# Kernel optimization log

Hardware: AMD Instinct MI355X
Metric: run time of the kernel (lower is better)

Reference implementation:

```python
import jax, jax.numpy as jnp
import numpy as np

N = 50000   # nodes
E = 800000  # edges (before self-loops)
IN, HID, OUT = 128, 128, 64


def gcn_norm(edge_index, num_nodes):
    # add self loops with weight 1, then symmetric deg^-1/2 normalization
    loop = jnp.arange(num_nodes, dtype=edge_index.dtype)
    row = jnp.concatenate([edge_index[0], loop])
    col = jnp.concatenate([edge_index[1], loop])
    ew = jnp.ones(row.shape[0], dtype=jnp.float32)
    deg = jax.ops.segment_sum(ew, col, num_segments=num_nodes)
    dis = jnp.where(deg > 0, jax.lax.rsqrt(deg), 0.0)
    norm = dis[row] * ew * dis[col]
    return row, col, norm


def gcn_conv(x, row, col, norm, W, b):
    h = x @ W                                   # [N, F_out] dense GEMM
    msg = h[row] * norm[:, None]                # gather + scale over edges
    out = jax.ops.segment_sum(msg, col, num_segments=x.shape[0])  # scatter-add
    return out + b


def setup_inputs() -> dict:
    key = jax.random.key(0)
    k0, k1, k2, k3, k4, k5 = jax.random.split(key, 6)
    x = jax.random.normal(k0, (N, IN), dtype=jnp.float32)
    edge_index = jax.random.randint(k1, (2, E), 0, N, dtype=jnp.int32)
    # glorot-style init for linear weights, zeros for bias (PyG default)
    W1 = jax.random.normal(k2, (IN, HID), dtype=jnp.float32) * np.float32(np.sqrt(1.0 / IN))
    b1 = jnp.zeros((HID,), dtype=jnp.float32)
    W2 = jax.random.normal(k3, (HID, OUT), dtype=jnp.float32) * np.float32(np.sqrt(1.0 / HID))
    b2 = jnp.zeros((OUT,), dtype=jnp.float32)
    return {"x": x, "edge_index": edge_index, "W1": W1, "b1": b1, "W2": W2, "b2": b2}


def reference(x, edge_index, W1, b1, W2, b2):
    row, col, norm = gcn_norm(edge_index, x.shape[0])
    h = jax.nn.relu(gcn_conv(x, row, col, norm, W1, b1))
    # dropout is a no-op in eval mode (training=False)
    out = gcn_conv(h, row, col, norm, W2, b2)
    return out
```

## Files before the change

### kernel.cpp

```cpp
#include <hip/hip_runtime.h>
#include <hip/hip_fp16.h>


#define Nn 50000
#define Ne 800000
#define NE2 (Ne / 2)
#define SCAN_B ((Nn + 1023) / 1024)
#define GT32 ((Nn + 31) / 32)
#define E1B ((NE2 + 255) / 256)

using f16x8 = _Float16 __attribute__((ext_vector_type(8)));
using f32x4 = float __attribute__((ext_vector_type(4)));

__global__ __launch_bounds__(256) void k_count_prep(
    const int2* __restrict__ col2, int* __restrict__ degi,
    ushort2* __restrict__ rank2, const float* __restrict__ W1,
    const float* __restrict__ W2, _Float16* __restrict__ W1h,
    _Float16* __restrict__ W2h) {
  const int b = blockIdx.x, t = threadIdx.x;
  if (b < E1B) {
    int i0 = b * 256 + t;
    if (i0 < NE2) {
      int2 c = col2[i0];
      ushort2 rk;
      rk.x = (unsigned short)atomicAdd(&degi[c.x], 1);
      rk.y = (unsigned short)atomicAdd(&degi[c.y], 1);
      rank2[i0] = rk;
    }
  } else if (b == E1B) {
    for (int i = 0; i < 8; ++i) {
      int id = i * 256 + t;
      int c = id & 127, k8 = id >> 7;
      f16x8 hv;
      #pragma unroll
      for (int j = 0; j < 8; ++j) hv[j] = (_Float16)W1[(k8 * 8 + j) * 128 + c];
      *(f16x8*)&W1h[c * 128 + ((k8 ^ (c & 7)) << 3)] = hv;
    }
  } else {
    for (int i = 0; i < 4; ++i) {
      int id = i * 256 + t;
      int c = id & 63, k8 = id >> 6;
      f16x8 hv;
      #pragma unroll
      for (int j = 0; j < 8; ++j) hv[j] = (_Float16)W2[(k8 * 8 + j) * 64 + c];
      *(f16x8*)&W2h[c * 128 + ((k8 ^ (c & 7)) << 3)] = hv;
    }
  }
}

__global__ __launch_bounds__(1024) void k_scan1(const int* __restrict__ degi,
                                                int* __restrict__ rowptr,
                                                float* __restrict__ dis,
                                                int* __restrict__ bsum) {
  __shared__ int wsum[16];
  int tid = threadIdx.x;
  int lane = tid & 63, wid = tid >> 6;
  int i = blockIdx.x * 1024 + tid;
  int v = (i < Nn) ? degi[i] : 0;
  if (i < Nn) dis[i] = rsqrtf((float)(v + 1));
  int incl = v;
  #pragma unroll
  for (int off = 1; off < 64; off <<= 1) {
    int t = __shfl_up(incl, off);
    if (lane >= off) incl += t;
  }
  if (lane == 63) wsum[wid] = incl;
  __syncthreads();
  if (wid == 0) {
    int wv = (lane < 16) ? wsum[lane] : 0;
    #pragma unroll
    for (int off = 1; off < 16; off <<= 1) {
      int t = __shfl_up(wv, off);
      if (lane >= off) wv += t;
    }
    if (lane < 16) wsum[lane] = wv;
  }
  __syncthreads();
  int woff = (wid > 0) ? wsum[wid - 1] : 0;
  if (i < Nn) rowptr[i] = woff + incl - v;
  if (tid == 0) bsum[blockIdx.x] = wsum[15];
}

__global__ __launch_bounds__(1024) void k_scan3(int* __restrict__ rowptr,
                                                const int* __restrict__ bsum) {
  __shared__ int off_s;
  int tid = threadIdx.x;
  if (tid < 64) {
    int v = (tid < SCAN_B) ? bsum[tid] : 0;
    int incl = v;
    #pragma unroll
    for (int off = 1; off < 64; off <<= 1) {
      int t = __shfl_up(incl, off);
      if (tid >= off) incl += t;
    }
    if (tid == (int)blockIdx.x) off_s = incl - v;
    if (blockIdx.x == 0 && tid == SCAN_B - 1) rowptr[Nn] = incl;
  }
  __syncthreads();
  int i = blockIdx.x * 1024 + tid;
  if (i < Nn) rowptr[i] += off_s;
}

__global__ __launch_bounds__(256, 5) void k_gemm32_fill(
    const float* __restrict__ X, const _Float16* __restrict__ W1h,
    const float* __restrict__ dis, __half* __restrict__ H,
    const int2* __restrict__ row2, const int2* __restrict__ col2,
    const int* __restrict__ rowptr, const ushort2* __restrict__ rank2,
    unsigned short* __restrict__ csr) {
  __shared__ _Float16 Wts[128 * 128];
  _Float16* Hsx = Wts;

  const int tid = threadIdx.x;
  const int base = blockIdx.x * 32;

  {
    const f16x8* src = (const f16x8*)W1h;
    f16x8* dst = (f16x8*)Wts;
    #pragma unroll
    for (int i = 0; i < 8; ++i) dst[i * 256 + tid] = src[i * 256 + tid];
  }

  {
    int t = blockIdx.x * 256 + tid;
    if (t < NE2) {
      int2 r = row2[t];
      int2 c = col2[t];
      ushort2 k = rank2[t];
      csr[rowptr[c.x] + (int)k.x] = (unsigned short)r.x;
      csr[rowptr[c.y] + (int)k.y] = (unsigned short)r.y;
    }
  }

  const int w = tid >> 6, lane = tid & 63;
  const int quad = lane >> 4, mrow = lane & 15;
  const int rbase = (w & 1) * 16, cbase = (w >> 1) * 64;
  int anode = base + rbase + mrow;
  if (anode >= Nn) anode = Nn - 1;
  const float4* xg = (const float4*)(X + (size_t)anode * 128);
  f16x8 av[4];
  #pragma unroll
  for (int ko = 0; ko < 4; ++ko) {
    float4 x0 = xg[ko * 8 + quad * 2];
    float4 x1 = xg[ko * 8 + quad * 2 + 1];
    av[ko][0] = (_Float16)x0.x; av[ko][1] = (_Float16)x0.y;
    av[ko][2] = (_Float16)x0.z; av[ko][3] = (_Float16)x0.w;
    av[ko][4] = (_Float16)x1.x; av[ko][5] = (_Float16)x1.y;
    av[ko][6] = (_Float16)x1.z; av[ko][7] = (_Float16)x1.w;
  }

  float dv[4];
  #pragma unroll
  for (int r = 0; r < 4; ++r) {
    int node = base + rbase + quad * 4 + r;
    dv[r] = dis[(node < Nn) ? node : (Nn - 1)];
  }
  __syncthreads();

  f32x4 acc[4];
  #pragma unroll
  for (int ct = 0; ct < 4; ++ct) acc[ct] = (f32x4){0.f, 0.f, 0.f, 0.f};

  #pragma unroll
  for (int ko = 0; ko < 4; ++ko) {
    #pragma unroll
    for (int ct = 0; ct < 4; ++ct) {
      int c = cbase + ct * 16 + mrow;
      f16x8 bv = *(const f16x8*)&Wts[c * 128 + (((ko * 4 + quad) ^ (c & 7)) << 3)];
      acc[ct] = __builtin_amdgcn_mfma_f32_16x16x32_f16(av[ko], bv, acc[ct], 0, 0, 0);
    }
  }

  __syncthreads();
  #pragma unroll
  for (int ct = 0; ct < 4; ++ct) {
    #pragma unroll
    for (int r = 0; r < 4; ++r)
      Hsx[(rbase + quad * 4 + r) * 136 + cbase + ct * 16 + mrow] =
          (_Float16)(acc[ct][r] * dv[r]);
  }
  __syncthreads();

  #pragma unroll
  for (int i = 0; i < 2; ++i) {
    int id = i * 256 + tid;
    int r = id >> 4, ch = id & 15;
    int node = base + r;
    if (node < Nn)
      *(f16x8*)((_Float16*)H + (size_t)node * 128 + ch * 8) =
          *(const f16x8*)&Hsx[r * 136 + ch * 8];
  }
}

__device__ __forceinline__ float2 h2f(unsigned int u) {
  return __half22float2(*(const __half2*)&u);
}

__global__ __launch_bounds__(256) void k_agg128_gemm64(
    const __half* __restrict__ H, const unsigned short* __restrict__ csr,
    const int* __restrict__ rowptr, const float* __restrict__ dis,
    const float* __restrict__ bias, const _Float16* __restrict__ W2h,
    __half* __restrict__ H2, int n) {
  __shared__ _Float16 Wts[64 * 128];
  __shared__ _Float16 Hs[16 * 136];

  const int tid = threadIdx.x;
  const int wid = tid >> 6, lane = tid & 63;
  const int sub = lane >> 4, fl = lane & 15;
  const int nb = wid * 4 + sub;
  const int v = blockIdx.x * 16 + nb;

  {
    const f16x8* src = (const f16x8*)W2h;
    f16x8* dst = (f16x8*)Wts;
    #pragma unroll
    for (int i = 0; i < 4; ++i) dst[i * 256 + tid] = src[i * 256 + tid];
  }

  int s = rowptr[v], e = rowptr[v + 1];
  float d = dis[v];
  const uint4* Hq = (const uint4*)H;
  uint4 hv = Hq[(size_t)v * 16 + fl];
  float2 p0 = h2f(hv.x), p1 = h2f(hv.y), p2 = h2f(hv.z), p3 = h2f(hv.w);
  float a0 = p0.x, a1 = p0.y, a2 = p1.x, a3 = p1.y;
  float a4 = p2.x, a5 = p2.y, a6 = p3.x, a7 = p3.y;
  constexpr int D = 8;
  if (s < e) {
    int srcs[D];
    #pragma unroll
    for (int j = 0; j < D; ++j) {
      int idx = s + j;
      srcs[j] = csr[(idx < e) ? idx : (e - 1)];
    }
    int base = s;
    for (; base + D <= e; base += D) {
      uint4 q[D];
      #pragma unroll
      for (int j = 0; j < D; ++j) q[j] = Hq[(size_t)srcs[j] * 16 + fl];
      int ns[D];
      #pragma unroll
      for (int j = 0; j < D; ++j) {
        int idx = base + D + j;
        ns[j] = csr[(idx < e) ? idx : (e - 1)];
      }
      #pragma unroll
      for (int j = 0; j < D; ++j) {
        float2 t;
        t = h2f(q[j].x); a0 += t.x; a1 += t.y;
        t = h2f(q[j].y); a2 += t.x; a3 += t.y;
        t = h2f(q[j].z); a4 += t.x; a5 += t.y;
        t = h2f(q[j].w); a6 += t.x; a7 += t.y;
      }
      #pragma unroll
      for (int j = 0; j < D; ++j) srcs[j] = ns[j];
    }
    if (base < e) {
      uint4 q[D];
      #pragma unroll
      for (int j = 0; j < D; ++j) q[j] = Hq[(size_t)srcs[j] * 16 + fl];
      #pragma unroll
      for (int j = 0; j < D; ++j) {
        float m = (base + j < e) ? 1.f : 0.f;
        float2 t;
        t = h2f(q[j].x); a0 = fmaf(m, t.x, a0); a1 = fmaf(m, t.y, a1);
        t = h2f(q[j].y); a2 = fmaf(m, t.x, a2); a3 = fmaf(m, t.y, a3);
        t = h2f(q[j].z); a4 = fmaf(m, t.x, a4); a5 = fmaf(m, t.y, a5);
        t = h2f(q[j].w); a6 = fmaf(m, t.x, a6); a7 = fmaf(m, t.y, a7);
      }
    }
  }
  {
    const float4* Bq = (const float4*)bias;
    float4 b0 = Bq[fl * 2], b1v = Bq[fl * 2 + 1];
    f16x8 hrow;
    hrow[0] = (_Float16)fmaxf(fmaf(d, a0, b0.x), 0.f);
    hrow[1] = (_Float16)fmaxf(fmaf(d, a1, b0.y), 0.f);
    hrow[2] = (_Float16)fmaxf(fmaf(d, a2, b0.z), 0.f);
    hrow[3] = (_Float16)fmaxf(fmaf(d, a3, b0.w), 0.f);
    hrow[4] = (_Float16)fmaxf(fmaf(d, a4, b1v.x), 0.f);
    hrow[5] = (_Float16)fmaxf(fmaf(d, a5, b1v.y), 0.f);
    hrow[6] = (_Float16)fmaxf(fmaf(d, a6, b1v.z), 0.f);
    hrow[7] = (_Float16)fmaxf(fmaf(d, a7, b1v.w), 0.f);
    *(f16x8*)&Hs[nb * 136 + fl * 8] = hrow;
  }

  const int quad = lane >> 4, mrow = lane & 15;
  float dst4[4];
  #pragma unroll
  for (int r = 0; r < 4; ++r)
    dst4[r] = dis[blockIdx.x * 16 + quad * 4 + r];
  __syncthreads();

  f32x4 acc = (f32x4){0.f, 0.f, 0.f, 0.f};
  const int c = wid * 16 + mrow;
  #pragma unroll
  for (int ko = 0; ko < 4; ++ko) {
    f16x8 avx = *(const f16x8*)&Hs[mrow * 136 + ko * 32 + quad * 8];
    f16x8 bv = *(const f16x8*)&Wts[c * 128 + (((ko * 4 + quad) ^ (c & 7)) << 3)];
    acc = __builtin_amdgcn_mfma_f32_16x16x32_f16(avx, bv, acc, 0, 0, 0);
  }

  __syncthreads();
  #pragma unroll
  for (int r = 0; r < 4; ++r)
    Hs[(quad * 4 + r) * 136 + wid * 16 + mrow] =
        (_Float16)(acc[r] * dst4[r]);
  __syncthreads();

  if (tid < 128) {
    int r = tid >> 3, ch = tid & 7;
    *(f16x8*)((_Float16*)H2 + ((size_t)blockIdx.x * 16 + r) * 64 + ch * 8) =
        *(const f16x8*)&Hs[r * 136 + ch * 8];
  }
}

__global__ __launch_bounds__(256) void k_agg64(const __half* __restrict__ H,
                                               const unsigned short* __restrict__ csr,
                                               const int* __restrict__ rowptr,
                                               const float* __restrict__ dis,
                                               const float* __restrict__ bias,
                                               float* __restrict__ Out, int n) {
  const int wid = threadIdx.x >> 6, lane = threadIdx.x & 63;
  const int sub = lane >> 4, fl = lane & 15;
  int v = blockIdx.x * 16 + wid * 4 + sub;
  if (v >= n) return;
  int s = rowptr[v], e = rowptr[v + 1];
  float d = dis[v];
  const uint2* Hq = (const uint2*)H;
  uint2 hv = Hq[(size_t)v * 16 + fl];
  float2 p0 = h2f(hv.x), p1 = h2f(hv.y);
  float a0 = p0.x, a1 = p0.y, a2 = p1.x, a3 = p1.y;
  constexpr int D = 8;
  if (s < e) {
    int srcs[D];
    #pragma unroll
    for (int j = 0; j < D; ++j) {
      int idx = s + j;
      srcs[j] = csr[(idx < e) ? idx : (e - 1)];
    }
    int base = s;
    for (; base + D <= e; base += D) {
      uint2 q[D];
      #pragma unroll
      for (int j = 0; j < D; ++j) q[j] = Hq[(size_t)srcs[j] * 16 + fl];
      int ns[D];
      #pragma unroll
      for (int j = 0; j < D; ++j) {
        int idx = base + D + j;
        ns[j] = csr[(idx < e) ? idx : (e - 1)];
      }
      #pragma unroll
      for (int j = 0; j < D; ++j) {
        float2 t;
        t = h2f(q[j].x); a0 += t.x; a1 += t.y;
        t = h2f(q[j].y); a2 += t.x; a3 += t.y;
      }
      #pragma unroll
      for (int j = 0; j < D; ++j) srcs[j] = ns[j];
    }
    if (base < e) {
      uint2 q[D];
      #pragma unroll
      for (int j = 0; j < D; ++j) q[j] = Hq[(size_t)srcs[j] * 16 + fl];
      #pragma unroll
      for (int j = 0; j < D; ++j) {
        float m = (base + j < e) ? 1.f : 0.f;
        float2 t;
        t = h2f(q[j].x); a0 = fmaf(m, t.x, a0); a1 = fmaf(m, t.y, a1);
        t = h2f(q[j].y); a2 = fmaf(m, t.x, a2); a3 = fmaf(m, t.y, a3);
      }
    }
  }
  const float4* Bq = (const float4*)bias;
  float4 b = Bq[fl];
  float4 o = make_float4(fmaf(d, a0, b.x), fmaf(d, a1, b.y),
                         fmaf(d, a2, b.z), fmaf(d, a3, b.w));
  ((float4*)(Out + (size_t)v * 64))[fl] = o;
}

extern "C" void kernel_launch(void* const* d_in, const int* in_sizes, int n_in,
                              void* d_out, int out_size, void* d_ws, size_t ws_size,
                              hipStream_t stream) {
  const float* x  = (const float*)d_in[0];
  const int*   ei = (const int*)d_in[1];
  const int*   row = ei;
  const int*   col = ei + Ne;
  const float* W1 = (const float*)d_in[2];
  const float* b1 = (const float*)d_in[3];
  const float* W2 = (const float*)d_in[4];
  const float* b2 = (const float*)d_in[5];
  float* out = (float*)d_out;

  char* ws = (char*)d_ws;
  size_t off = 0;
  auto alloc = [&](size_t bytes) -> void* {
    void* p = ws + off;
    off += (bytes + 255) & ~(size_t)255;
    return p;
  };
  int*    degi   = (int*)   alloc(Nn * sizeof(int));
  int*    rowptr = (int*)   alloc((Nn + 1) * sizeof(int));
  float*  dis    = (float*) alloc(Nn * sizeof(float));
  int*    bsum   = (int*)   alloc(64 * sizeof(int));
  unsigned short* rank = (unsigned short*)alloc((size_t)Ne * sizeof(unsigned short));
  unsigned short* csr  = (unsigned short*)alloc((size_t)Ne * sizeof(unsigned short));
  __half* H1     = (__half*)alloc((size_t)Nn * 128 * sizeof(__half));
  __half* H2     = (__half*)alloc((size_t)Nn * 64 * sizeof(__half));
  _Float16* W1h  = (_Float16*)alloc(128 * 128 * sizeof(_Float16));
  _Float16* W2h  = (_Float16*)alloc(64 * 128 * sizeof(_Float16));

  const int NGB = (Nn + 15) / 16;

  hipMemsetAsync(degi, 0, Nn * sizeof(int), stream);

  k_count_prep<<<E1B + 2, 256, 0, stream>>>((const int2*)col, degi,
                                            (ushort2*)rank, W1, W2, W1h, W2h);
  k_scan1<<<SCAN_B, 1024, 0, stream>>>(degi, rowptr, dis, bsum);
  k_scan3<<<SCAN_B, 1024, 0, stream>>>(rowptr, bsum);
  k_gemm32_fill<<<GT32, 256, 0, stream>>>(x, W1h, dis, H1, (const int2*)row,
                                          (const int2*)col, rowptr,
                                          (const ushort2*)rank, csr);
  k_agg128_gemm64<<<NGB, 256, 0, stream>>>(H1, csr, rowptr, dis, b1, W2h, H2, Nn);
  k_agg64<<<NGB, 256, 0, stream>>>(H2, csr, rowptr, dis, b2, out, Nn);
}
```

Baseline: 185.9 us.

## Split each node's edge list across two lane groups in both aggregation kernels

Both aggregation kernels now assign two 16-lane groups to each destination node. Each group handles alternate edges, and the partial sums are combined with a cross-lane xor shuffle. The first kernel moves to 512-thread blocks, with only four waves running the MFMA step. The second kernel processes 8 nodes per block. The aim is more memory-level parallelism on the gather-bound aggregations, halving per-thread serial latency chains. The cost is extra shuffles, idle waves during the GEMM, and strided index loads.

```diff
diff --git a/kernel.cpp b/kernel.cpp
--- a/kernel.cpp
+++ b/kernel.cpp
@@ -195,7 +195,7 @@
   return __half22float2(*(const __half2*)&u);
 }
 
-__global__ __launch_bounds__(256) void k_agg128_gemm64(
+__global__ __launch_bounds__(512) void k_agg128_gemm64(
     const __half* __restrict__ H, const unsigned short* __restrict__ csr,
     const int* __restrict__ rowptr, const float* __restrict__ dis,
     const float* __restrict__ bias, const _Float16* __restrict__ W2h,
@@ -204,42 +204,49 @@
   __shared__ _Float16 Hs[16 * 136];
 
   const int tid = threadIdx.x;
-  const int wid = tid >> 6, lane = tid & 63;
-  const int sub = lane >> 4, fl = lane & 15;
-  const int nb = wid * 4 + sub;
-  const int v = blockIdx.x * 16 + nb;
 
   {
     const f16x8* src = (const f16x8*)W2h;
     f16x8* dst = (f16x8*)Wts;
     #pragma unroll
-    for (int i = 0; i < 4; ++i) dst[i * 256 + tid] = src[i * 256 + tid];
-  }
+    for (int i = 0; i < 2; ++i) dst[i * 512 + tid] = src[i * 512 + tid];
+  }
+
+  const int nb = tid >> 5;
+  const int eg = (tid >> 4) & 1;
+  const int fl = tid & 15;
+  const int v = blockIdx.x * 16 + nb;
 
   int s = rowptr[v], e = rowptr[v + 1];
   float d = dis[v];
   const uint4* Hq = (const uint4*)H;
-  uint4 hv = Hq[(size_t)v * 16 + fl];
-  float2 p0 = h2f(hv.x), p1 = h2f(hv.y), p2 = h2f(hv.z), p3 = h2f(hv.w);
-  float a0 = p0.x, a1 = p0.y, a2 = p1.x, a3 = p1.y;
-  float a4 = p2.x, a5 = p2.y, a6 = p3.x, a7 = p3.y;
+  float a0 = 0.f, a1 = 0.f, a2 = 0.f, a3 = 0.f;
+  float a4 = 0.f, a5 = 0.f, a6 = 0.f, a7 = 0.f;
+  if (eg == 0) {
+    uint4 hv = Hq[(size_t)v * 16 + fl];
+    float2 p0 = h2f(hv.x), p1 = h2f(hv.y), p2 = h2f(hv.z), p3 = h2f(hv.w);
+    a0 = p0.x; a1 = p0.y; a2 = p1.x; a3 = p1.y;
+    a4 = p2.x; a5 = p2.y; a6 = p3.x; a7 = p3.y;
+  }
+  const int cnt = (e - s + 1 - eg) >> 1;
+  const int pos = s + eg;
   constexpr int D = 8;
-  if (s < e) {
+  if (cnt > 0) {
     int srcs[D];
     #pragma unroll
     for (int j = 0; j < D; ++j) {
-      int idx = s + j;
+      int idx = pos + 2 * j;
       srcs[j] = csr[(idx < e) ? idx : (e - 1)];
     }
-    int base = s;
-    for (; base + D <= e; base += D) {
+    int done = 0;
+    for (; done + D <= cnt; done += D) {
       uint4 q[D];
       #pragma unroll
       for (int j = 0; j < D; ++j) q[j] = Hq[(size_t)srcs[j] * 16 + fl];
       int ns[D];
       #pragma unroll
       for (int j = 0; j < D; ++j) {
-        int idx = base + D + j;
+        int idx = pos + 2 * (done + D + j);
         ns[j] = csr[(idx < e) ? idx : (e - 1)];
       }
       #pragma unroll
@@ -253,13 +260,13 @@
       #pragma unroll
       for (int j = 0; j < D; ++j) srcs[j] = ns[j];
     }
-    if (base < e) {
+    if (done < cnt) {
       uint4 q[D];
       #pragma unroll
       for (int j = 0; j < D; ++j) q[j] = Hq[(size_t)srcs[j] * 16 + fl];
       #pragma unroll
       for (int j = 0; j < D; ++j) {
-        float m = (base + j < e) ? 1.f : 0.f;
+        float m = (done + j < cnt) ? 1.f : 0.f;
         float2 t;
         t = h2f(q[j].x); a0 = fmaf(m, t.x, a0); a1 = fmaf(m, t.y, a1);
         t = h2f(q[j].y); a2 = fmaf(m, t.x, a2); a3 = fmaf(m, t.y, a3);
@@ -268,7 +275,12 @@
       }
     }
   }
-  {
+  a0 += __shfl_xor(a0, 16); a1 += __shfl_xor(a1, 16);
+  a2 += __shfl_xor(a2, 16); a3 += __shfl_xor(a3, 16);
+  a4 += __shfl_xor(a4, 16); a5 += __shfl_xor(a5, 16);
+  a6 += __shfl_xor(a6, 16); a7 += __shfl_xor(a7, 16);
+
+  if (eg == 0) {
     const float4* Bq = (const float4*)bias;
     float4 b0 = Bq[fl * 2], b1v = Bq[fl * 2 + 1];
     f16x8 hrow;
@@ -283,27 +295,33 @@
     *(f16x8*)&Hs[nb * 136 + fl * 8] = hrow;
   }
 
+  const int wid = tid >> 6, lane = tid & 63;
   const int quad = lane >> 4, mrow = lane & 15;
   float dst4[4];
-  #pragma unroll
-  for (int r = 0; r < 4; ++r)
-    dst4[r] = dis[blockIdx.x * 16 + quad * 4 + r];
+  if (wid < 4) {
+    #pragma unroll
+    for (int r = 0; r < 4; ++r)
+      dst4[r] = dis[blockIdx.x * 16 + quad * 4 + r];
+  }
   __syncthreads();
 
   f32x4 acc = (f32x4){0.f, 0.f, 0.f, 0.f};
-  const int c = wid * 16 + mrow;
-  #pragma unroll
-  for (int ko = 0; ko < 4; ++ko) {
-    f16x8 avx = *(const f16x8*)&Hs[mrow * 136 + ko * 32 + quad * 8];
-    f16x8 bv = *(const f16x8*)&Wts[c * 128 + (((ko * 4 + quad) ^ (c & 7)) << 3)];
-    acc = __builtin_amdgcn_mfma_f32_16x16x32_f16(avx, bv, acc, 0, 0, 0);
-  }
-
-  __syncthreads();
-  #pragma unroll
-  for (int r = 0; r < 4; ++r)
-    Hs[(quad * 4 + r) * 136 + wid * 16 + mrow] =
-        (_Float16)(acc[r] * dst4[r]);
+  if (wid < 4) {
+    const int c = wid * 16 + mrow;
+    #pragma unroll
+    for (int ko = 0; ko < 4; ++ko) {
+      f16x8 avx = *(const f16x8*)&Hs[mrow * 136 + ko * 32 + quad * 8];
+      f16x8 bv = *(const f16x8*)&Wts[c * 128 + (((ko * 4 + quad) ^ (c & 7)) << 3)];
+      acc = __builtin_amdgcn_mfma_f32_16x16x32_f16(avx, bv, acc, 0, 0, 0);
+    }
+  }
+  __syncthreads();
+  if (wid < 4) {
+    #pragma unroll
+    for (int r = 0; r < 4; ++r)
+      Hs[(quad * 4 + r) * 136 + wid * 16 + mrow] =
+          (_Float16)(acc[r] * dst4[r]);
+  }
   __syncthreads();
 
   if (tid < 128) {
@@ -319,33 +337,39 @@
                                                const float* __restrict__ dis,
                                                const float* __restrict__ bias,
                                                float* __restrict__ Out, int n) {
-  const int wid = threadIdx.x >> 6, lane = threadIdx.x & 63;
-  const int sub = lane >> 4, fl = lane & 15;
-  int v = blockIdx.x * 16 + wid * 4 + sub;
-  if (v >= n) return;
+  const int tid = threadIdx.x;
+  const int nb = tid >> 5;
+  const int eg = (tid >> 4) & 1;
+  const int fl = tid & 15;
+  const int v = blockIdx.x * 8 + nb;
   int s = rowptr[v], e = rowptr[v + 1];
   float d = dis[v];
   const uint2* Hq = (const uint2*)H;
-  uint2 hv = Hq[(size_t)v * 16 + fl];
-  float2 p0 = h2f(hv.x), p1 = h2f(hv.y);
-  float a0 = p0.x, a1 = p0.y, a2 = p1.x, a3 = p1.y;
+  float a0 = 0.f, a1 = 0.f, a2 = 0.f, a3 = 0.f;
+  if (eg == 0) {
+    uint2 hv = Hq[(size_t)v * 16 + fl];
+    float2 p0 = h2f(hv.x), p1 = h2f(hv.y);
+    a0 = p0.x; a1 = p0.y; a2 = p1.x; a3 = p1.y;
+  }
+  const int cnt = (e - s + 1 - eg) >> 1;
+  const int pos = s + eg;
   constexpr int D = 8;
-  if (s < e) {
+  if (cnt > 0) {
     int srcs[D];
     #pragma unroll
     for (int j = 0; j < D; ++j) {
-      int idx = s + j;
+      int idx = pos + 2 * j;
       srcs[j] = csr[(idx < e) ? idx : (e - 1)];
     }
-    int base = s;
-    for (; base + D <= e; base += D) {
+    int done = 0;
+    for (; done + D <= cnt; done += D) {
       uint2 q[D];
       #pragma unroll
       for (int j = 0; j < D; ++j) q[j] = Hq[(size_t)srcs[j] * 16 + fl];
       int ns[D];
       #pragma unroll
       for (int j = 0; j < D; ++j) {
-        int idx = base + D + j;
+        int idx = pos + 2 * (done + D + j);
         ns[j] = csr[(idx < e) ? idx : (e - 1)];
       }
       #pragma unroll
@@ -357,24 +381,28 @@
       #pragma unroll
       for (int j = 0; j < D; ++j) srcs[j] = ns[j];
     }
-    if (base < e) {
+    if (done < cnt) {
       uint2 q[D];
       #pragma unroll
       for (int j = 0; j < D; ++j) q[j] = Hq[(size_t)srcs[j] * 16 + fl];
       #pragma unroll
       for (int j = 0; j < D; ++j) {
-        float m = (base + j < e) ? 1.f : 0.f;
+        float m = (done + j < cnt) ? 1.f : 0.f;
         float2 t;
         t = h2f(q[j].x); a0 = fmaf(m, t.x, a0); a1 = fmaf(m, t.y, a1);
         t = h2f(q[j].y); a2 = fmaf(m, t.x, a2); a3 = fmaf(m, t.y, a3);
       }
     }
   }
-  const float4* Bq = (const float4*)bias;
-  float4 b = Bq[fl];
-  float4 o = make_float4(fmaf(d, a0, b.x), fmaf(d, a1, b.y),
-                         fmaf(d, a2, b.z), fmaf(d, a3, b.w));
-  ((float4*)(Out + (size_t)v * 64))[fl] = o;
+  a0 += __shfl_xor(a0, 16); a1 += __shfl_xor(a1, 16);
+  a2 += __shfl_xor(a2, 16); a3 += __shfl_xor(a3, 16);
+  if (eg == 0) {
+    const float4* Bq = (const float4*)bias;
+    float4 b = Bq[fl];
+    float4 o = make_float4(fmaf(d, a0, b.x), fmaf(d, a1, b.y),
+                           fmaf(d, a2, b.z), fmaf(d, a3, b.w));
+    ((float4*)(Out + (size_t)v * 64))[fl] = o;
+  }
 }
 
 extern "C" void kernel_launch(void* const* d_in, const int* in_sizes, int n_in,
@@ -409,6 +437,7 @@
   _Float16* W2h  = (_Float16*)alloc(64 * 128 * sizeof(_Float16));
 
   const int NGB = (Nn + 15) / 16;
+  const int NGB8 = (Nn + 7) / 8;
 
   hipMemsetAsync(degi, 0, Nn * sizeof(int), stream);
 
@@ -419,6 +448,6 @@
   k_gemm32_fill<<<GT32, 256, 0, stream>>>(x, W1h, dis, H1, (const int2*)row,
                                           (const int2*)col, rowptr,
                                           (const ushort2*)rank, csr);
-  k_agg128_gemm64<<<NGB, 256, 0, stream>>>(H1, csr, rowptr, dis, b1, W2h, H2, Nn);
-  k_agg64<<<NGB, 256, 0, stream>>>(H2, csr, rowptr, dis, b2, out, Nn);
-}
+  k_agg128_gemm64<<<NGB, 512, 0, stream>>>(H1, csr, rowptr, dis, b1, W2h, H2, Nn);
+  k_agg64<<<NGB8, 256, 0, stream>>>(H2, csr, rowptr, dis, b2, out, Nn);
+}
```

Measured after the change: 192.1 us. +3.4%, slower.
